# Optimization experiments

Hardware: AMD Instinct MI355X
Metric: run time of the kernel (lower is better)

The kernel has to match this reference:

```python
import jax, jax.numpy as jnp
import numpy as np

B, L, DM, H = 2, 4096, 1024, 16
D = DM // H


def setup_inputs() -> dict:
    key = jax.random.key(0)
    ks = jax.random.split(key, 11)
    s = 1.0 / np.sqrt(DM)
    return {
        "query": jax.random.normal(ks[0], (B, L, DM), jnp.float32),
        "key": jax.random.normal(ks[1], (B, L, DM), jnp.float32),
        "value": jax.random.normal(ks[2], (B, L, DM), jnp.float32),
        "Wq": jax.random.normal(ks[3], (DM, DM), jnp.float32) * s,
        "bq": jnp.zeros((DM,), jnp.float32),
        "Wk": jax.random.normal(ks[4], (DM, DM), jnp.float32) * s,
        "bk": jnp.zeros((DM,), jnp.float32),
        "Wv": jax.random.normal(ks[5], (DM, DM), jnp.float32) * s,
        "bv": jnp.zeros((DM,), jnp.float32),
        "Wo": jax.random.normal(ks[6], (DM, DM), jnp.float32) * s,
        "bo": jnp.zeros((DM,), jnp.float32),
    }


def _split_heads(x):
    # (B, L, DM) -> (B, H, L, D)
    b, l, _ = x.shape
    return x.reshape(b, l, H, D).transpose(0, 2, 1, 3)


def reference(query, key, value, Wq, bq, Wk, bk, Wv, bv, Wo, bo):
    q = _split_heads(query @ Wq + bq)
    k = _split_heads(key @ Wk + bk)
    v = _split_heads(value @ Wv + bv)
    # ELU+1 feature map
    q = jax.nn.elu(q) + 1.0
    k = jax.nn.elu(k) + 1.0
    # Original: kv = einsum('bhld,bhmd->bhlm', k, v); out = einsum('bhlm,bhld->bhmd', kv, q)
    # Equivalent (associativity): out[m,d] = sum_e v[m,e] * (sum_l k[l,e] q[l,d])
    S = jnp.einsum('bhle,bhld->bhed', k, q)          # (B,H,D,D)
    out = jnp.einsum('bhme,bhed->bhmd', v, S)        # (B,H,L,D)
    denom = jnp.einsum('bhld,bhld->bhl', q, k) + 1e-6
    out = out / denom[..., None]
    # combine heads: (B,H,L,D) -> (B,L,DM)
    out = out.transpose(0, 2, 1, 3).reshape(out.shape[0], -1, DM)
    # out_dense; dropout is identity at inference
    return out @ Wo + bo
```

## Files before the change

### kernel.cpp

```cpp
#include <hip/hip_runtime.h>

#define B_  2
#define L_  4096
#define DM_ 1024
#define H_  16
#define D_  64
#define M_  (B_ * L_)

typedef unsigned short u16;
typedef short bf16x8 __attribute__((ext_vector_type(8)));
typedef float f32x4  __attribute__((ext_vector_type(4)));

typedef const __attribute__((address_space(1))) void* as1_cvp;
typedef __attribute__((address_space(3))) void* as3_vp;

__device__ __forceinline__ float b2f(u16 u) {
    union { unsigned int i; float f; } x; x.i = ((unsigned int)u) << 16; return x.f;
}
__device__ __forceinline__ u16 f2b(float f) {
    unsigned int x = __float_as_uint(f);
    return (u16)((x + 0x7fffu + ((x >> 16) & 1u)) >> 16);
}

__global__ void cast_bf16_kernel(const float* __restrict__ in, u16* __restrict__ out, int n4) {
    int i = blockIdx.x * blockDim.x + threadIdx.x;
    if (i < n4) {
        float4 v = ((const float4*)in)[i];
        ushort4 o;
        o.x = f2b(v.x); o.y = f2b(v.y); o.z = f2b(v.z); o.w = f2b(v.w);
        ((ushort4*)out)[i] = o;
    }
}

__global__ void transpose_cast_kernel(const float* __restrict__ W, u16* __restrict__ Wt) {
    __shared__ float tile[32][33];
    int tx = threadIdx.x, ty = threadIdx.y;
    int n = blockIdx.x * 32 + tx;
    int k0 = blockIdx.y * 32;
#pragma unroll
    for (int i = 0; i < 4; ++i)
        tile[ty + i * 8][tx] = W[(size_t)(k0 + ty + i * 8) * DM_ + n];
    __syncthreads();
#pragma unroll
    for (int i = 0; i < 4; ++i) {
        int nn = blockIdx.x * 32 + ty + i * 8;
        Wt[(size_t)nn * DM_ + k0 + tx] = f2b(tile[tx][ty + i * 8]);
    }
}

__global__ void zero_f32_kernel(float* __restrict__ p, int n) {
    int i = blockIdx.x * blockDim.x + threadIdx.x;
    if (i < n) p[i] = 0.f;
}

template <int MODE, bool ELU>
__global__ __launch_bounds__(256, 3) void gemm_bt_kernel(
    const u16* __restrict__ A, const u16* __restrict__ Bt,
    const float* __restrict__ bias, void* __restrict__ Cout,
    int M, int N, int K)
{
    __shared__ __align__(16) u16 smem[MODE == 2 ? 17408 : 16384];
    u16* As = smem;
    u16* Bs = smem + 8192;

    const int t    = threadIdx.x;
    const int lane = t & 63;
    const int wave = t >> 6;
    const int wr   = wave >> 1;
    const int wc   = wave & 1;
    const int quad = lane >> 4;
    const int l16  = lane & 15;
    const int m0   = blockIdx.x * 128;
    const int n0   = blockIdx.y * 128;

    f32x4 acc[4][4] = {};

    for (int kt = 0; kt < K; kt += 64) {
#pragma unroll
        for (int i = 0; i < 4; ++i) {
            int c   = i * 256 + t;
            int row = c >> 3;
            int kc  = c & 7;
            int cbase = i * 256 + wave * 64;
            const u16* gA = A  + (size_t)(m0 + row) * K + kt + kc * 8;
            const u16* gB = Bt + (size_t)(n0 + row) * K + kt + kc * 8;
            __builtin_amdgcn_global_load_lds((as1_cvp)gA, (as3_vp)(As + cbase * 8), 16, 0, 0);
            __builtin_amdgcn_global_load_lds((as1_cvp)gB, (as3_vp)(Bs + cbase * 8), 16, 0, 0);
        }
        __syncthreads();
#pragma unroll
        for (int ks = 0; ks < 2; ++ks) {
            bf16x8 af[4], bfr[4];
#pragma unroll
            for (int it = 0; it < 4; ++it)
                af[it] = *(const bf16x8*)(As + (wr * 64 + it * 16 + l16) * 64 + ks * 32 + quad * 8);
#pragma unroll
            for (int jt = 0; jt < 4; ++jt)
                bfr[jt] = *(const bf16x8*)(Bs + (wc * 64 + jt * 16 + l16) * 64 + ks * 32 + quad * 8);
#pragma unroll
            for (int it = 0; it < 4; ++it)
#pragma unroll
                for (int jt = 0; jt < 4; ++jt)
                    acc[it][jt] = __builtin_amdgcn_mfma_f32_16x16x32_bf16(
                        af[it], bfr[jt], acc[it][jt], 0, 0, 0);
        }
        __syncthreads();
    }

    if (MODE != 2) {
#pragma unroll
        for (int it = 0; it < 4; ++it) {
            int row0 = m0 + wr * 64 + it * 16 + quad * 4;
#pragma unroll
            for (int jt = 0; jt < 4; ++jt) {
                int col = n0 + wc * 64 + jt * 16 + l16;
                float bv = bias[col];
#pragma unroll
                for (int r = 0; r < 4; ++r) {
                    float x = acc[it][jt][r] + bv;
                    if (ELU) x = (x > 0.f) ? (x + 1.f) : __expf(x);
                    if (MODE == 1)
                        ((u16*)Cout)[(size_t)(row0 + r) * N + col] = f2b(x);
                    else
                        ((float*)Cout)[(size_t)(row0 + r) * N + col] = x;
                }
            }
        }
    } else {
        u16* Ct = smem;
#pragma unroll
        for (int it = 0; it < 4; ++it) {
            int row0 = wr * 64 + it * 16 + quad * 4;
#pragma unroll
            for (int jt = 0; jt < 4; ++jt) {
                int colr = wc * 64 + jt * 16 + l16;
                float bv = bias[n0 + colr];
                ushort4 o;
                float x0 = acc[it][jt][0] + bv;
                float x1 = acc[it][jt][1] + bv;
                float x2 = acc[it][jt][2] + bv;
                float x3 = acc[it][jt][3] + bv;
                if (ELU) {
                    x0 = (x0 > 0.f) ? (x0 + 1.f) : __expf(x0);
                    x1 = (x1 > 0.f) ? (x1 + 1.f) : __expf(x1);
                    x2 = (x2 > 0.f) ? (x2 + 1.f) : __expf(x2);
                    x3 = (x3 > 0.f) ? (x3 + 1.f) : __expf(x3);
                }
                o.x = f2b(x0); o.y = f2b(x1); o.z = f2b(x2); o.w = f2b(x3);
                *(ushort4*)&Ct[colr * 136 + row0] = o;
            }
        }
        __syncthreads();
        int b   = m0 >> 12;
        int seg = t & 15;
        int cg  = t >> 4;
#pragma unroll
        for (int iter = 0; iter < 8; ++iter) {
            int colIdx = iter * 16 + cg;
            int gcol = n0 + colIdx;
            int bh = b * 16 + (gcol >> 6);
            int e  = gcol & 63;
            uint4 v = *(const uint4*)&Ct[colIdx * 136 + seg * 8];
            *(uint4*)((u16*)Cout + ((size_t)bh << 18) + ((size_t)e << 12)
                      + (m0 & 4095) + seg * 8) = v;
        }
    }
}

__global__ __launch_bounds__(256) void attn_s_kernel(
    const u16* __restrict__ QpT, const u16* __restrict__ KpT,
    float* __restrict__ S, float* __restrict__ denom)
{
    const int t    = threadIdx.x;
    const int lane = t & 63;
    const int wave = t >> 6;
    const int quad = lane >> 4;
    const int l16  = lane & 15;
    const int bh   = blockIdx.x;
    const int lc   = blockIdx.y * 256;

    const u16* baseQ = QpT + ((size_t)bh << 18);
    const u16* baseK = KpT + ((size_t)bh << 18);

    f32x4 acc[4] = {};
    const u16* arow = baseK + (size_t)(wave * 16 + l16) * 4096 + lc;
#pragma unroll
    for (int ks = 0; ks < 8; ++ks) {
        int koff = ks * 32 + quad * 8;
        bf16x8 a = *(const bf16x8*)(arow + koff);
#pragma unroll
        for (int dt = 0; dt < 4; ++dt) {
            bf16x8 b = *(const bf16x8*)(baseQ + (size_t)(dt * 16 + l16) * 4096 + lc + koff);
            acc[dt] = __builtin_amdgcn_mfma_f32_16x16x32_bf16(a, b, acc[dt], 0, 0, 0);
        }
    }
    float* Sb = S + (size_t)bh * 4096;
#pragma unroll
    for (int dt = 0; dt < 4; ++dt)
#pragma unroll
        for (int r = 0; r < 4; ++r)
            atomicAdd(&Sb[(wave * 16 + quad * 4 + r) * 64 + dt * 16 + l16], acc[dt][r]);

    if (t < 128) {
        float s0 = 0.f, s1 = 0.f;
        int off = lc + 2 * t;
#pragma unroll 8
        for (int e = 0; e < 64; ++e) {
            unsigned int qv = *(const unsigned int*)(baseQ + (size_t)e * 4096 + off);
            unsigned int kv = *(const unsigned int*)(baseK + (size_t)e * 4096 + off);
            s0 += b2f((u16)(qv & 0xffff)) * b2f((u16)(kv & 0xffff));
            s1 += b2f((u16)(qv >> 16))   * b2f((u16)(kv >> 16));
        }
        denom[(size_t)bh * 4096 + off]     = s0 + 1e-6f;
        denom[(size_t)bh * 4096 + off + 1] = s1 + 1e-6f;
    }
}

__global__ __launch_bounds__(256) void attn_out_kernel(
    const u16* __restrict__ Vp, const float* __restrict__ S,
    const float* __restrict__ denom, u16* __restrict__ ctx)
{
    __shared__ __align__(16) u16 Sb[64 * 64];
    __shared__ float dsh[256];
    const int t    = threadIdx.x;
    const int lane = t & 63;
    const int wave = t >> 6;
    const int quad = lane >> 4;
    const int l16  = lane & 15;
    const int bh   = blockIdx.x;
    const int b    = bh >> 4, h = bh & 15;
    const int lc   = blockIdx.y * 256;

    {
        const float* Sg = S + (size_t)bh * 4096;
        int e = t >> 2, d0 = (t & 3) * 16;
#pragma unroll
        for (int i = 0; i < 16; ++i)
            Sb[(d0 + i) * 64 + e] = f2b(Sg[e * 64 + d0 + i]);
        dsh[t] = denom[(size_t)bh * 4096 + lc + t];
    }
    __syncthreads();

    const u16* Abase = Vp + (size_t)b * L_ * DM_ + (size_t)(lc + wave * 64 + l16) * DM_ + h * 64;
    f32x4 acc[4][4] = {};
#pragma unroll
    for (int ks = 0; ks < 2; ++ks) {
        int koff = ks * 32 + quad * 8;
        bf16x8 af[4], bfr[4];
#pragma unroll
        for (int lt = 0; lt < 4; ++lt)
            af[lt] = *(const bf16x8*)(Abase + (size_t)(lt * 16) * DM_ + koff);
#pragma unroll
        for (int dt = 0; dt < 4; ++dt)
            bfr[dt] = *(const bf16x8*)(Sb + (dt * 16 + l16) * 64 + koff);
#pragma unroll
        for (int lt = 0; lt < 4; ++lt)
#pragma unroll
            for (int dt = 0; dt < 4; ++dt)
                acc[lt][dt] = __builtin_amdgcn_mfma_f32_16x16x32_bf16(
                    af[lt], bfr[dt], acc[lt][dt], 0, 0, 0);
    }

    u16* cbase = ctx + (size_t)b * L_ * DM_ + h * 64;
#pragma unroll
    for (int lt = 0; lt < 4; ++lt) {
        int lrow0 = wave * 64 + lt * 16 + quad * 4;
        float inv[4];
#pragma unroll
        for (int r = 0; r < 4; ++r) inv[r] = 1.f / dsh[lrow0 + r];
#pragma unroll
        for (int dt = 0; dt < 4; ++dt) {
            int d = dt * 16 + l16;
#pragma unroll
            for (int r = 0; r < 4; ++r)
                cbase[(size_t)(lc + lrow0 + r) * DM_ + d] = f2b(acc[lt][dt][r] * inv[r]);
        }
    }
}

extern "C" void kernel_launch(void* const* d_in, const int* in_sizes, int n_in,
                              void* d_out, int out_size, void* d_ws, size_t ws_size,
                              hipStream_t stream)
{
    const float* query = (const float*)d_in[0];
    const float* key   = (const float*)d_in[1];
    const float* value = (const float*)d_in[2];
    const float* Wq = (const float*)d_in[3];  const float* bq = (const float*)d_in[4];
    const float* Wk = (const float*)d_in[5];  const float* bk = (const float*)d_in[6];
    const float* Wv = (const float*)d_in[7];  const float* bv = (const float*)d_in[8];
    const float* Wo = (const float*)d_in[9];  const float* bo = (const float*)d_in[10];

    const size_t SZ = (size_t)M_ * DM_ * sizeof(u16);
    char* ws = (char*)d_ws;
    u16* qb  = (u16*)(ws + 0 * SZ);
    u16* kb  = (u16*)(ws + 1 * SZ);
    u16* vb  = (u16*)(ws + 2 * SZ);
    u16* QpT = (u16*)(ws + 3 * SZ);
    u16* KpT = (u16*)(ws + 4 * SZ);
    u16* Vp  = qb;
    u16* ctx = kb;
    u16* Wqt = (u16*)(ws + 5 * SZ);
    u16* Wkt = Wqt + (size_t)DM_ * DM_;
    u16* Wvt = Wkt + (size_t)DM_ * DM_;
    u16* Wot = Wvt + (size_t)DM_ * DM_;
    float* S     = (float*)(ws + 5 * SZ + 4 * (size_t)DM_ * DM_ * sizeof(u16));
    float* denom = S + (size_t)B_ * H_ * D_ * D_;

    dim3 tb(32, 8), tg(32, 32);
    transpose_cast_kernel<<<tg, tb, 0, stream>>>(Wq, Wqt);
    transpose_cast_kernel<<<tg, tb, 0, stream>>>(Wk, Wkt);
    transpose_cast_kernel<<<tg, tb, 0, stream>>>(Wv, Wvt);
    transpose_cast_kernel<<<tg, tb, 0, stream>>>(Wo, Wot);

    int n4 = M_ * DM_ / 4;
    cast_bf16_kernel<<<n4 / 256, 256, 0, stream>>>(query, qb, n4);
    cast_bf16_kernel<<<n4 / 256, 256, 0, stream>>>(key,   kb, n4);
    cast_bf16_kernel<<<n4 / 256, 256, 0, stream>>>(value, vb, n4);

    int nS = B_ * H_ * D_ * D_;
    zero_f32_kernel<<<nS / 256, 256, 0, stream>>>(S, nS);

    dim3 gg(M_ / 128, DM_ / 128);
    gemm_bt_kernel<2, true ><<<gg, 256, 0, stream>>>(qb, Wqt, bq, QpT, M_, DM_, DM_);
    gemm_bt_kernel<2, true ><<<gg, 256, 0, stream>>>(kb, Wkt, bk, KpT, M_, DM_, DM_);
    gemm_bt_kernel<1, false><<<gg, 256, 0, stream>>>(vb, Wvt, bv, Vp, M_, DM_, DM_);

    attn_s_kernel<<<dim3(B_ * H_, L_ / 256), 256, 0, stream>>>(QpT, KpT, S, denom);

    attn_out_kernel<<<dim3(B_ * H_, L_ / 256), 256, 0, stream>>>(Vp, S, denom, ctx);

    gemm_bt_kernel<0, false><<<gg, 256, 0, stream>>>(ctx, Wot, bo, (float*)d_out, M_, DM_, DM_);
}
```

Before: 321.3 us.

## Batch QKV GEMMs, casts and transposes into single launches; enlarge attn_s tiles

The three input casts, four weight transposes and three projection GEMMs each become one launch, with the operand picked by blockIdx.z. This cuts launch count and lets the QKV GEMM fill the GPU with three times as many blocks in a single wave set. attn_s now covers 512 positions per block, so there are half as many atomicAdds into S, and all 256 threads compute the denominator. Vp and ctx move to separate workspace buffers, which is needed because qb and kb are still being read while the batched GEMM runs.

New measurement: 285.6 us. 1.13x faster.

```diff
diff --git a/kernel.cpp b/kernel.cpp
--- a/kernel.cpp
+++ b/kernel.cpp
@@ -22,7 +22,13 @@
     return (u16)((x + 0x7fffu + ((x >> 16) & 1u)) >> 16);
 }
 
-__global__ void cast_bf16_kernel(const float* __restrict__ in, u16* __restrict__ out, int n4) {
+__global__ void cast3_bf16_kernel(const float* __restrict__ i0, const float* __restrict__ i1,
+                                  const float* __restrict__ i2,
+                                  u16* __restrict__ o0, u16* __restrict__ o1, u16* __restrict__ o2,
+                                  int n4) {
+    int z = blockIdx.z;
+    const float* in = z == 0 ? i0 : (z == 1 ? i1 : i2);
+    u16* out       = z == 0 ? o0 : (z == 1 ? o1 : o2);
     int i = blockIdx.x * blockDim.x + threadIdx.x;
     if (i < n4) {
         float4 v = ((const float4*)in)[i];
@@ -32,7 +38,13 @@
     }
 }
 
-__global__ void transpose_cast_kernel(const float* __restrict__ W, u16* __restrict__ Wt) {
+__global__ void transpose4_cast_kernel(const float* __restrict__ w0, const float* __restrict__ w1,
+                                       const float* __restrict__ w2, const float* __restrict__ w3,
+                                       u16* __restrict__ t0, u16* __restrict__ t1,
+                                       u16* __restrict__ t2, u16* __restrict__ t3) {
+    int z = blockIdx.z;
+    const float* W = z == 0 ? w0 : z == 1 ? w1 : z == 2 ? w2 : w3;
+    u16* Wt        = z == 0 ? t0 : z == 1 ? t1 : z == 2 ? t2 : t3;
     __shared__ float tile[32][33];
     int tx = threadIdx.x, ty = threadIdx.y;
     int n = blockIdx.x * 32 + tx;
@@ -53,13 +65,18 @@
     if (i < n) p[i] = 0.f;
 }
 
-template <int MODE, bool ELU>
-__global__ __launch_bounds__(256, 3) void gemm_bt_kernel(
-    const u16* __restrict__ A, const u16* __restrict__ Bt,
-    const float* __restrict__ bias, void* __restrict__ Cout,
-    int M, int N, int K)
+__global__ __launch_bounds__(256, 3) void gemm_qkv_kernel(
+    const u16* __restrict__ qb, const u16* __restrict__ kb, const u16* __restrict__ vb,
+    const u16* __restrict__ Wqt, const u16* __restrict__ Wkt, const u16* __restrict__ Wvt,
+    const float* __restrict__ bq, const float* __restrict__ bk, const float* __restrict__ bv,
+    u16* __restrict__ QpT, u16* __restrict__ KpT, u16* __restrict__ Vp)
 {
-    __shared__ __align__(16) u16 smem[MODE == 2 ? 17408 : 16384];
+    const int z = blockIdx.z;
+    const u16* A    = z == 0 ? qb  : z == 1 ? kb  : vb;
+    const u16* Bt   = z == 0 ? Wqt : z == 1 ? Wkt : Wvt;
+    const float* bias = z == 0 ? bq : z == 1 ? bk : bv;
+
+    __shared__ __align__(16) u16 smem[17408];
     u16* As = smem;
     u16* Bs = smem + 8192;
 
@@ -72,6 +89,7 @@
     const int l16  = lane & 15;
     const int m0   = blockIdx.x * 128;
     const int n0   = blockIdx.y * 128;
+    const int K    = DM_;
 
     f32x4 acc[4][4] = {};
 
@@ -107,26 +125,21 @@
         __syncthreads();
     }
 
-    if (MODE != 2) {
+    if (z == 2) {
 #pragma unroll
         for (int it = 0; it < 4; ++it) {
             int row0 = m0 + wr * 64 + it * 16 + quad * 4;
 #pragma unroll
             for (int jt = 0; jt < 4; ++jt) {
                 int col = n0 + wc * 64 + jt * 16 + l16;
-                float bv = bias[col];
-#pragma unroll
-                for (int r = 0; r < 4; ++r) {
-                    float x = acc[it][jt][r] + bv;
-                    if (ELU) x = (x > 0.f) ? (x + 1.f) : __expf(x);
-                    if (MODE == 1)
-                        ((u16*)Cout)[(size_t)(row0 + r) * N + col] = f2b(x);
-                    else
-                        ((float*)Cout)[(size_t)(row0 + r) * N + col] = x;
-                }
+                float bv2 = bias[col];
+#pragma unroll
+                for (int r = 0; r < 4; ++r)
+                    Vp[(size_t)(row0 + r) * DM_ + col] = f2b(acc[it][jt][r] + bv2);
             }
         }
     } else {
+        u16* OutT = z == 0 ? QpT : KpT;
         u16* Ct = smem;
 #pragma unroll
         for (int it = 0; it < 4; ++it) {
@@ -134,18 +147,16 @@
 #pragma unroll
             for (int jt = 0; jt < 4; ++jt) {
                 int colr = wc * 64 + jt * 16 + l16;
-                float bv = bias[n0 + colr];
+                float bv2 = bias[n0 + colr];
+                float x0 = acc[it][jt][0] + bv2;
+                float x1 = acc[it][jt][1] + bv2;
+                float x2 = acc[it][jt][2] + bv2;
+                float x3 = acc[it][jt][3] + bv2;
+                x0 = (x0 > 0.f) ? (x0 + 1.f) : __expf(x0);
+                x1 = (x1 > 0.f) ? (x1 + 1.f) : __expf(x1);
+                x2 = (x2 > 0.f) ? (x2 + 1.f) : __expf(x2);
+                x3 = (x3 > 0.f) ? (x3 + 1.f) : __expf(x3);
                 ushort4 o;
-                float x0 = acc[it][jt][0] + bv;
-                float x1 = acc[it][jt][1] + bv;
-                float x2 = acc[it][jt][2] + bv;
-                float x3 = acc[it][jt][3] + bv;
-                if (ELU) {
-                    x0 = (x0 > 0.f) ? (x0 + 1.f) : __expf(x0);
-                    x1 = (x1 > 0.f) ? (x1 + 1.f) : __expf(x1);
-                    x2 = (x2 > 0.f) ? (x2 + 1.f) : __expf(x2);
-                    x3 = (x3 > 0.f) ? (x3 + 1.f) : __expf(x3);
-                }
                 o.x = f2b(x0); o.y = f2b(x1); o.z = f2b(x2); o.w = f2b(x3);
                 *(ushort4*)&Ct[colr * 136 + row0] = o;
             }
@@ -161,8 +172,75 @@
             int bh = b * 16 + (gcol >> 6);
             int e  = gcol & 63;
             uint4 v = *(const uint4*)&Ct[colIdx * 136 + seg * 8];
-            *(uint4*)((u16*)Cout + ((size_t)bh << 18) + ((size_t)e << 12)
+            *(uint4*)(OutT + ((size_t)bh << 18) + ((size_t)e << 12)
                       + (m0 & 4095) + seg * 8) = v;
+        }
+    }
+}
+
+__global__ __launch_bounds__(256, 3) void gemm_out_kernel(
+    const u16* __restrict__ A, const u16* __restrict__ Bt,
+    const float* __restrict__ bias, float* __restrict__ Cout)
+{
+    __shared__ __align__(16) u16 smem[16384];
+    u16* As = smem;
+    u16* Bs = smem + 8192;
+
+    const int t    = threadIdx.x;
+    const int lane = t & 63;
+    const int wave = t >> 6;
+    const int wr   = wave >> 1;
+    const int wc   = wave & 1;
+    const int quad = lane >> 4;
+    const int l16  = lane & 15;
+    const int m0   = blockIdx.x * 128;
+    const int n0   = blockIdx.y * 128;
+    const int K    = DM_;
+
+    f32x4 acc[4][4] = {};
+
+    for (int kt = 0; kt < K; kt += 64) {
+#pragma unroll
+        for (int i = 0; i < 4; ++i) {
+            int c   = i * 256 + t;
+            int row = c >> 3;
+            int kc  = c & 7;
+            int cbase = i * 256 + wave * 64;
+            const u16* gA = A  + (size_t)(m0 + row) * K + kt + kc * 8;
+            const u16* gB = Bt + (size_t)(n0 + row) * K + kt + kc * 8;
+            __builtin_amdgcn_global_load_lds((as1_cvp)gA, (as3_vp)(As + cbase * 8), 16, 0, 0);
+            __builtin_amdgcn_global_load_lds((as1_cvp)gB, (as3_vp)(Bs + cbase * 8), 16, 0, 0);
+        }
+        __syncthreads();
+#pragma unroll
+        for (int ks = 0; ks < 2; ++ks) {
+            bf16x8 af[4], bfr[4];
+#pragma unroll
+            for (int it = 0; it < 4; ++it)
+                af[it] = *(const bf16x8*)(As + (wr * 64 + it * 16 + l16) * 64 + ks * 32 + quad * 8);
+#pragma unroll
+            for (int jt = 0; jt < 4; ++jt)
+                bfr[jt] = *(const bf16x8*)(Bs + (wc * 64 + jt * 16 + l16) * 64 + ks * 32 + quad * 8);
+#pragma unroll
+            for (int it = 0; it < 4; ++it)
+#pragma unroll
+                for (int jt = 0; jt < 4; ++jt)
+                    acc[it][jt] = __builtin_amdgcn_mfma_f32_16x16x32_bf16(
+                        af[it], bfr[jt], acc[it][jt], 0, 0, 0);
+        }
+        __syncthreads();
+    }
+
+#pragma unroll
+    for (int it = 0; it < 4; ++it) {
+        int row0 = m0 + wr * 64 + it * 16 + quad * 4;
+#pragma unroll
+        for (int jt = 0; jt < 4; ++jt) {
+            int col = n0 + wc * 64 + jt * 16 + l16;
+            float bv = bias[col];
+#pragma unroll
+            for (int r = 0; r < 4; ++r)
+                Cout[(size_t)(row0 + r) * DM_ + col] = acc[it][jt][r] + bv;
         }
     }
 }
@@ -177,15 +255,15 @@
     const int quad = lane >> 4;
     const int l16  = lane & 15;
     const int bh   = blockIdx.x;
-    const int lc   = blockIdx.y * 256;
+    const int lc   = blockIdx.y * 512;
 
     const u16* baseQ = QpT + ((size_t)bh << 18);
     const u16* baseK = KpT + ((size_t)bh << 18);
 
     f32x4 acc[4] = {};
     const u16* arow = baseK + (size_t)(wave * 16 + l16) * 4096 + lc;
-#pragma unroll
-    for (int ks = 0; ks < 8; ++ks) {
+#pragma unroll 4
+    for (int ks = 0; ks < 16; ++ks) {
         int koff = ks * 32 + quad * 8;
         bf16x8 a = *(const bf16x8*)(arow + koff);
 #pragma unroll
@@ -201,7 +279,7 @@
         for (int r = 0; r < 4; ++r)
             atomicAdd(&Sb[(wave * 16 + quad * 4 + r) * 64 + dt * 16 + l16], acc[dt][r]);
 
-    if (t < 128) {
+    {
         float s0 = 0.f, s1 = 0.f;
         int off = lc + 2 * t;
 #pragma unroll 8
@@ -305,29 +383,27 @@
     u16* Wot = Wvt + (size_t)DM_ * DM_;
     float* S     = (float*)(ws + 5 * SZ + 4 * (size_t)DM_ * DM_ * sizeof(u16));
     float* denom = S + (size_t)B_ * H_ * D_ * D_;
-
-    dim3 tb(32, 8), tg(32, 32);
-    transpose_cast_kernel<<<tg, tb, 0, stream>>>(Wq, Wqt);
-    transpose_cast_kernel<<<tg, tb, 0, stream>>>(Wk, Wkt);
-    transpose_cast_kernel<<<tg, tb, 0, stream>>>(Wv, Wvt);
-    transpose_cast_kernel<<<tg, tb, 0, stream>>>(Wo, Wot);
+    u16* Vp2  = (u16*)((char*)(denom + (size_t)B_ * H_ * L_) + 256);
+    u16* ctx2 = (u16*)((char*)Vp2 + SZ);
+    Vp = Vp2; ctx = ctx2;
+
+    transpose4_cast_kernel<<<dim3(32, 32, 4), dim3(32, 8), 0, stream>>>(
+        Wq, Wk, Wv, Wo, Wqt, Wkt, Wvt, Wot);
 
     int n4 = M_ * DM_ / 4;
-    cast_bf16_kernel<<<n4 / 256, 256, 0, stream>>>(query, qb, n4);
-    cast_bf16_kernel<<<n4 / 256, 256, 0, stream>>>(key,   kb, n4);
-    cast_bf16_kernel<<<n4 / 256, 256, 0, stream>>>(value, vb, n4);
+    cast3_bf16_kernel<<<dim3(n4 / 256, 1, 3), 256, 0, stream>>>(
+        query, key, value, qb, kb, vb, n4);
 
     int nS = B_ * H_ * D_ * D_;
     zero_f32_kernel<<<nS / 256, 256, 0, stream>>>(S, nS);
 
-    dim3 gg(M_ / 128, DM_ / 128);
-    gemm_bt_kernel<2, true ><<<gg, 256, 0, stream>>>(qb, Wqt, bq, QpT, M_, DM_, DM_);
-    gemm_bt_kernel<2, true ><<<gg, 256, 0, stream>>>(kb, Wkt, bk, KpT, M_, DM_, DM_);
-    gemm_bt_kernel<1, false><<<gg, 256, 0, stream>>>(vb, Wvt, bv, Vp, M_, DM_, DM_);
-
-    attn_s_kernel<<<dim3(B_ * H_, L_ / 256), 256, 0, stream>>>(QpT, KpT, S, denom);
+    gemm_qkv_kernel<<<dim3(M_ / 128, DM_ / 128, 3), 256, 0, stream>>>(
+        qb, kb, vb, Wqt, Wkt, Wvt, bq, bk, bv, QpT, KpT, Vp);
+
+    attn_s_kernel<<<dim3(B_ * H_, L_ / 512), 256, 0, stream>>>(QpT, KpT, S, denom);
 
     attn_out_kernel<<<dim3(B_ * H_, L_ / 256), 256, 0, stream>>>(Vp, S, denom, ctx);
 
-    gemm_bt_kernel<0, false><<<gg, 256, 0, stream>>>(ctx, Wot, bo, (float*)d_out, M_, DM_, DM_);
-}
+    gemm_out_kernel<<<dim3(M_ / 128, DM_ / 128), 256, 0, stream>>>(
+        ctx, Wot, bo, (float*)d_out);
+}
```
